# Optimization experiments

Measured on AMD Instinct MI355X. Metric: run time of the kernel, lower is better.

Reference implementation:

```python
import jax, jax.numpy as jnp
import numpy as np

# Fixed average-trace buffer from the module (length 120)
AVG = jnp.asarray([0.0256,0.0823,0.1157,0.1315,0.1366,0.1369,0.1347,0.1308,0.1259,0.1205,0.1146,0.1086,0.1028,0.097,0.0913,0.0858,0.0805,0.0756,0.0708,0.0664,0.0623,0.0584,0.0549,0.0515,0.0485,0.0456,0.0429,0.0404,0.0381,0.036,0.034,0.0321,0.0304,0.0287,0.0272,0.0258,0.0245,0.0233,0.0222,0.0211,0.0201,0.0191,0.0182,0.0173,0.0165,0.0158,0.015,0.0143,0.0137,0.013,0.0125,0.0119,0.0114,0.0108,0.0104,0.0099,0.0095,0.0091,0.0087,0.0083,0.008,0.0077,0.0074,0.0071,0.0068,0.0065,0.0062,0.006,0.0058,0.0055,0.0053,0.005,0.0049,0.0047,0.0045,0.0044,0.0042,0.004,0.0039,0.0038,0.0036,0.0034,0.0033,0.0032,0.0031,0.003,0.0029,0.0028,0.0027,0.0026,0.0025,0.0024,0.0023,0.0022,0.0021,0.0021,0.002,0.0019,0.0018,0.0018,0.0017,0.0017,0.0016,0.0016,0.0015,0.0015,0.0014,0.0014,0.0013,0.0013,0.0013,0.0012,0.0012,0.0011,0.0011,0.0011,0.001,0.001,0.001,0.0009], dtype=jnp.float32)


def _lstm(x, w_ih, w_hh, b):
    """PyTorch-semantics single-layer LSTM. x: [N,T,D], w_ih: [4H,D], w_hh: [4H,H], b: [4H] (= b_ih + b_hh). Gate order i,f,g,o."""
    xp = jnp.einsum('ntd,gd->ntg', x, w_ih) + b  # precompute input projections: [N,T,4H]
    N = x.shape[0]
    H = w_hh.shape[1]
    h0 = jnp.zeros((N, H), x.dtype)

    def step(carry, xt):
        h, c = carry
        g = xt + h @ w_hh.T  # [N,4H]
        i, f, gg, o = jnp.split(g, 4, axis=-1)
        c = jax.nn.sigmoid(f) * c + jax.nn.sigmoid(i) * jnp.tanh(gg)
        h = jax.nn.sigmoid(o) * jnp.tanh(c)
        return (h, c), h

    _, hs = jax.lax.scan(step, (h0, h0), jnp.swapaxes(xp, 0, 1))  # hs: [T,N,H]
    return jnp.swapaxes(hs, 0, 1)  # [N,T,H]


def setup_inputs() -> dict:
    key = jax.random.key(0)
    ks = jax.random.split(key, 7)
    N, F, H = 32768, 12, 30
    s1 = 1.0 / float(np.sqrt(H))  # torch LSTM init: U(-1/sqrt(H), 1/sqrt(H))
    s2 = 1.0                      # second LSTM hidden=1 -> scale 1
    return {
        'features': jax.random.normal(ks[0], (N, F), jnp.float32),
        'w_ih1': jax.random.uniform(ks[1], (4 * H, F + 1), jnp.float32, -s1, s1),
        'w_hh1': jax.random.uniform(ks[2], (4 * H, H), jnp.float32, -s1, s1),
        'b1': jax.random.uniform(ks[3], (4 * H,), jnp.float32, -s1, s1),
        'w_ih2': jax.random.uniform(ks[4], (4, H), jnp.float32, -s2, s2),
        'w_hh2': jax.random.uniform(ks[5], (4, 1), jnp.float32, -s2, s2),
        'b2': jax.random.uniform(ks[6], (4,), jnp.float32, -s2, s2),
    }


def reference(features, w_ih1, w_hh1, b1, w_ih2, w_hh2, b2):
    N, F = features.shape
    T = AVG.shape[0]  # 120
    x = jnp.broadcast_to(features[:, None, :], (N, T, F))          # repeat features over time
    trace = jnp.broadcast_to(AVG[None, :, None], (N, T, 1))        # average trace channel
    x = jnp.concatenate([x, trace], axis=2)                        # [N,120,13]
    h1 = _lstm(x, w_ih1, w_hh1, b1)                                # [N,120,30]
    return _lstm(h1, w_ih2, w_hh2, b2)                             # [N,120,1]
```

## Files before the change

kernel.cpp:

```cpp
#include <hip/hip_runtime.h>

typedef __attribute__((ext_vector_type(8))) short bf16x8;
typedef __attribute__((ext_vector_type(4))) float f32x4;

#define LOG2E 1.44269504088896340736f

__device__ __constant__ float AVG_D[120] = {
    0.0256f,0.0823f,0.1157f,0.1315f,0.1366f,0.1369f,0.1347f,0.1308f,0.1259f,0.1205f,
    0.1146f,0.1086f,0.1028f,0.0970f,0.0913f,0.0858f,0.0805f,0.0756f,0.0708f,0.0664f,
    0.0623f,0.0584f,0.0549f,0.0515f,0.0485f,0.0456f,0.0429f,0.0404f,0.0381f,0.0360f,
    0.0340f,0.0321f,0.0304f,0.0287f,0.0272f,0.0258f,0.0245f,0.0233f,0.0222f,0.0211f,
    0.0201f,0.0191f,0.0182f,0.0173f,0.0165f,0.0158f,0.0150f,0.0143f,0.0137f,0.0130f,
    0.0125f,0.0119f,0.0114f,0.0108f,0.0104f,0.0099f,0.0095f,0.0091f,0.0087f,0.0083f,
    0.0080f,0.0077f,0.0074f,0.0071f,0.0068f,0.0065f,0.0062f,0.0060f,0.0058f,0.0055f,
    0.0053f,0.0050f,0.0049f,0.0047f,0.0045f,0.0044f,0.0042f,0.0040f,0.0039f,0.0038f,
    0.0036f,0.0034f,0.0033f,0.0032f,0.0031f,0.0030f,0.0029f,0.0028f,0.0027f,0.0026f,
    0.0025f,0.0024f,0.0023f,0.0022f,0.0021f,0.0021f,0.0020f,0.0019f,0.0018f,0.0018f,
    0.0017f,0.0017f,0.0016f,0.0016f,0.0015f,0.0015f,0.0014f,0.0014f,0.0013f,0.0013f,
    0.0013f,0.0012f,0.0012f,0.0011f,0.0011f,0.0011f,0.0010f,0.0010f,0.0010f,0.0009f
};

__device__ __forceinline__ float sig2(float x) {
    return __builtin_amdgcn_rcpf(1.0f + __builtin_amdgcn_exp2f(x));
}
__device__ __forceinline__ float tanh2(float x) {
    return fmaf(2.0f, __builtin_amdgcn_rcpf(1.0f + __builtin_amdgcn_exp2f(x)), -1.0f);
}
__device__ __forceinline__ unsigned short tb(float x) {
    return (unsigned short)(__float_as_uint(x) >> 16);
}
__device__ __forceinline__ float fb(unsigned short h) {
    return __uint_as_float(((unsigned)h) << 16);
}

__device__ __forceinline__ void swap32(unsigned &a, unsigned &b) {
    auto r = __builtin_amdgcn_permlane32_swap(a, b, false, false);
    a = r[0]; b = r[1];
}
__device__ __forceinline__ void swap16(unsigned &a, unsigned &b) {
    auto r = __builtin_amdgcn_permlane16_swap(a, b, false, false);
    a = r[0]; b = r[1];
}

__global__ void pack_weights(const float* __restrict__ w_ih1,
                             const float* __restrict__ w_hh1,
                             const float* __restrict__ b1,
                             const float* __restrict__ w_ih2,
                             const float* __restrict__ b2,
                             float* __restrict__ ws) {
    unsigned short* whi = (unsigned short*)ws;
    unsigned short* wlo = (unsigned short*)(ws + 2048);
    float* bconst = ws + 4096;
    float* wih1f  = ws + 4224;
    unsigned* avgpk = (unsigned*)(ws + 5760);
    const int tid = threadIdx.x;
    for (int idx = tid; idx < 4096; idx += 256) {
        const int T = idx >> 9, lane = (idx >> 3) & 63, j = idx & 7;
        const int r = 16 * T + (lane & 15);
        const int k = ((lane >> 4) & 3) * 8 + j;
        const int u = r >> 2, q = r & 3;
        const float sc = (q == 2) ? (-2.0f * LOG2E) : (-LOG2E);
        float v = 0.0f;
        if (u < 30) {
            if (k < 30)       v = w_hh1[(q * 30 + u) * 30 + k];
            else if (k == 30) v = w_ih1[(q * 30 + u) * 13 + 12];
        } else if (u == 30 && k < 30) {
            v = w_ih2[q * 30 + k];
        }
        v *= sc;
        const unsigned short hi = tb(v);
        whi[idx] = hi;
        wlo[idx] = tb(v - fb(hi));
    }
    for (int r = tid; r < 128; r += 256) {
        const int u = r >> 2, q = r & 3;
        const float sc = (q == 2) ? (-2.0f * LOG2E) : (-LOG2E);
        bconst[r] = sc * ((u < 30) ? b1[q * 30 + u] : ((u == 30) ? b2[q] : 0.0f));
    }
    for (int idx = tid; idx < 1536; idx += 256) {
        const int r = idx / 12, d = idx % 12;
        const int u = r >> 2, q = r & 3;
        const float sc = (q == 2) ? (-2.0f * LOG2E) : (-LOG2E);
        wih1f[idx] = (u < 30) ? sc * w_ih1[(q * 30 + u) * 13 + d] : 0.0f;
    }
    for (int t = tid; t < 121; t += 256) {
        const float a = (t < 120) ? AVG_D[t] : 0.0f;
        const unsigned short hi = tb(a);
        const unsigned short lo = tb(a - fb(hi));
        avgpk[t] = (unsigned)hi | ((unsigned)lo << 16);
    }
}

__global__ __launch_bounds__(128, 2)
void lstm_mfma_kernel(const float* __restrict__ feat,
                      const float* __restrict__ w_hh2,
                      const float* __restrict__ ws,
                      float* __restrict__ out) {
    __shared__ __align__(16) float out_s[32 * 124];

    const int tid  = threadIdx.x;
    const int lane = tid & 63;
    const int wv   = __builtin_amdgcn_readfirstlane(tid >> 6);
    const int s    = lane & 15;
    const int quad = lane >> 4;
    const int seq  = blockIdx.x * 32 + wv * 16 + s;
    const unsigned* avgpk = (const unsigned*)(ws + 5760);

    bf16x8 Ahi[8], Alo[8];
    {
        const unsigned short* whi = (const unsigned short*)ws;
        const unsigned short* wlo = (const unsigned short*)(ws + 2048);
#pragma unroll
        for (int T = 0; T < 8; T++) {
            Ahi[T] = *(const bf16x8*)(whi + T * 512 + lane * 8);
            Alo[T] = *(const bf16x8*)(wlo + T * 512 + lane * 8);
        }
    }

    float f0[12];
    {
        const float4* fp = reinterpret_cast<const float4*>(feat + seq * 12);
        float4 A = fp[0], B = fp[1], C = fp[2];
        f0[0]=A.x; f0[1]=A.y; f0[2]=A.z; f0[3]=A.w;
        f0[4]=B.x; f0[5]=B.y; f0[6]=B.z; f0[7]=B.w;
        f0[8]=C.x; f0[9]=C.y; f0[10]=C.z; f0[11]=C.w;
    }
    f32x4 projb[8];
    {
        const float* bconst = ws + 4096;
        const float* wih1f  = ws + 4224;
#pragma unroll
        for (int T = 0; T < 8; T++) {
#pragma unroll
            for (int g = 0; g < 4; g++) {
                const int r = 16 * T + 4 * quad + g;
                float acc = bconst[r];
#pragma unroll
                for (int d = 0; d < 12; d++) acc = fmaf(f0[d], wih1f[r * 12 + d], acc);
                projb[T][g] = acc;
            }
        }
    }

    float c1[8];
#pragma unroll
    for (int T = 0; T < 8; T++) c1[T] = 0.0f;
    float h2 = 0.0f, c2 = 0.0f;
    const float whs0 = -LOG2E * w_hh2[0];
    const float whs1 = -LOG2E * w_hh2[1];
    const float whs2 = -2.0f * LOG2E * w_hh2[2];
    const float whs3 = -LOG2E * w_hh2[3];

    unsigned e0 = 0u, e1 = 0u, e2 = 0u, e3 = 0u;
    unsigned o0 = 0u, o1 = 0u, o2 = 0u, o3 = 0u;
    if (quad == 3) o2 = avgpk[0];
    union { int4 i; bf16x8 v; } ubh, ubl;
#define BUILD_B() do {                                                  \
        ubh.i.x = (int)__builtin_amdgcn_perm(e1, e0, 0x05040100u);      \
        ubh.i.y = (int)__builtin_amdgcn_perm(e3, e2, 0x05040100u);      \
        ubh.i.z = (int)__builtin_amdgcn_perm(o1, o0, 0x05040100u);      \
        ubh.i.w = (int)__builtin_amdgcn_perm(o3, o2, 0x05040100u);      \
        ubl.i.x = (int)__builtin_amdgcn_perm(e1, e0, 0x07060302u);      \
        ubl.i.y = (int)__builtin_amdgcn_perm(e3, e2, 0x07060302u);      \
        ubl.i.z = (int)__builtin_amdgcn_perm(o1, o0, 0x07060302u);      \
        ubl.i.w = (int)__builtin_amdgcn_perm(o3, o2, 0x07060302u);      \
    } while (0)
    BUILD_B();

    unsigned apk_cur = avgpk[1];

#pragma unroll 1
    for (int t = 0; t <= 120; t++) {
        const bf16x8 Bhi = ubh.v, Blo = ubl.v;

        const unsigned apk = apk_cur;
        apk_cur = avgpk[(t + 2 <= 120) ? (t + 2) : 120];

        f32x4 D[8];
#pragma unroll
        for (int T = 0; T < 8; T++)
            D[T] = __builtin_amdgcn_mfma_f32_16x16x32_bf16(Alo[T], Bhi, projb[T], 0, 0, 0);
#pragma unroll
        for (int T = 0; T < 8; T++)
            D[T] = __builtin_amdgcn_mfma_f32_16x16x32_bf16(Ahi[T], Blo, D[T], 0, 0, 0);
#pragma unroll
        for (int T = 0; T < 8; T++)
            D[T] = __builtin_amdgcn_mfma_f32_16x16x32_bf16(Ahi[T], Bhi, D[T], 0, 0, 0);

        if (t >= 1 && quad == 2) {
            const float g0 = fmaf(h2, whs0, D[7][0]);
            const float g1 = fmaf(h2, whs1, D[7][1]);
            const float g2 = fmaf(h2, whs2, D[7][2]);
            const float g3 = fmaf(h2, whs3, D[7][3]);
            c2 = sig2(g1) * c2 + sig2(g0) * tanh2(g2);
            h2 = sig2(g3) * tanh2(c2 * (-2.0f * LOG2E));
            out_s[(wv * 16 + s) * 124 + (t - 1)] = h2;
        }

        if (t < 120) {
            unsigned hpk[8];
#pragma unroll
            for (int T = 0; T < 8; T++) {
                const int u = 4 * T + quad;
                unsigned v = 0u;
                if (u < 30) {
                    const float ei = __builtin_amdgcn_exp2f(D[T][0]);
                    const float ef = __builtin_amdgcn_exp2f(D[T][1]);
                    const float eg = __builtin_amdgcn_exp2f(D[T][2]);
                    const float eo = __builtin_amdgcn_exp2f(D[T][3]);
                    const float pi_ = 1.0f + ei, pf = 1.0f + ef;
                    const float pg  = 1.0f + eg, po = 1.0f + eo;
                    const float pig = pi_ * pg;
                    const float num = fmaf(c1[T], pig, (1.0f - eg) * pf);
                    const float ck  = num * __builtin_amdgcn_rcpf(pf * pig);
                    c1[T] = ck;
                    float carg = -2.0f * LOG2E * ck;
                    carg = fminf(fmaxf(carg, -80.0f), 80.0f);
                    const float ec = __builtin_amdgcn_exp2f(carg);
                    const float hk = (1.0f - ec) *
                                     __builtin_amdgcn_rcpf(po * (1.0f + ec));
                    const unsigned hbits = __float_as_uint(hk);
                    const float rem = hk - __uint_as_float(hbits & 0xffff0000u);
                    v = __builtin_amdgcn_perm(__float_as_uint(rem), hbits, 0x07060302u);
                }
                hpk[T] = v;
            }

            e0 = hpk[0]; e1 = hpk[2]; e2 = hpk[4]; e3 = hpk[6];
            o0 = hpk[1]; o1 = hpk[3]; o2 = hpk[5]; o3 = hpk[7];
            swap32(e0, e2); swap32(e1, e3);
            swap16(e0, e1); swap16(e2, e3);
            swap32(o0, o2); swap32(o1, o3);
            swap16(o0, o1); swap16(o2, o3);
            if (quad == 3) { o2 = apk; o3 = 0u; }
            BUILD_B();
        }
    }

    __syncthreads();
    float* outb = out + (size_t)blockIdx.x * 32 * 120;
#pragma unroll
    for (int it = 0; it < 8; it++) {
        const int fi = it * 128 + tid;
        if (fi < 960) {
            const int sq = fi / 30, j = fi % 30;
            const float4 v = *reinterpret_cast<const float4*>(&out_s[sq * 124 + j * 4]);
            *reinterpret_cast<float4*>(&outb[sq * 120 + j * 4]) = v;
        }
    }
}

extern "C" void kernel_launch(void* const* d_in, const int* in_sizes, int n_in,
                              void* d_out, int out_size, void* d_ws, size_t ws_size,
                              hipStream_t stream) {
    (void)in_sizes; (void)n_in; (void)out_size; (void)ws_size;
    const float* feat  = (const float*)d_in[0];
    const float* w_ih1 = (const float*)d_in[1];
    const float* w_hh1 = (const float*)d_in[2];
    const float* b1    = (const float*)d_in[3];
    const float* w_ih2 = (const float*)d_in[4];
    const float* w_hh2 = (const float*)d_in[5];
    const float* b2    = (const float*)d_in[6];
    float* ws  = (float*)d_ws;
    float* out = (float*)d_out;

    hipLaunchKernelGGL(pack_weights, dim3(1), dim3(256), 0, stream,
                       w_ih1, w_hh1, b1, w_ih2, b2, ws);
    hipLaunchKernelGGL(lstm_mfma_kernel, dim3(1024), dim3(128), 0, stream,
                       feat, w_hh2, ws, out);
}
```

Before: 290.4 us.

## Split LSTM gate tiles across two waves with LDS hidden-state exchange

Each block now handles 16 sequences instead of 32, and its two waves each compute half of the 8 gate tiles. The hidden state is exchanged each timestep through a double-buffered LDS array guarded by __syncthreads, replacing the in-register permlane swaps. This halves per-wave MFMA and transcendental work per step and raises the occupancy hint, shortening the serial critical path. In exchange it adds an LDS round trip and a block barrier on every one of the 120 steps.

```diff
diff --git a/kernel.cpp b/kernel.cpp
--- a/kernel.cpp
+++ b/kernel.cpp
@@ -31,15 +31,6 @@
 }
 __device__ __forceinline__ float fb(unsigned short h) {
     return __uint_as_float(((unsigned)h) << 16);
-}
-
-__device__ __forceinline__ void swap32(unsigned &a, unsigned &b) {
-    auto r = __builtin_amdgcn_permlane32_swap(a, b, false, false);
-    a = r[0]; b = r[1];
-}
-__device__ __forceinline__ void swap16(unsigned &a, unsigned &b) {
-    auto r = __builtin_amdgcn_permlane16_swap(a, b, false, false);
-    a = r[0]; b = r[1];
 }
 
 __global__ void pack_weights(const float* __restrict__ w_ih1,
@@ -91,29 +82,35 @@
     }
 }
 
-__global__ __launch_bounds__(128, 2)
+__global__ __launch_bounds__(128, 4)
 void lstm_mfma_kernel(const float* __restrict__ feat,
                       const float* __restrict__ w_hh2,
                       const float* __restrict__ ws,
                       float* __restrict__ out) {
-    __shared__ __align__(16) float out_s[32 * 124];
+    __shared__ __align__(16) unsigned hx[2][16 * 36];
+    __shared__ __align__(16) float out_s[16 * 124];
 
     const int tid  = threadIdx.x;
     const int lane = tid & 63;
     const int wv   = __builtin_amdgcn_readfirstlane(tid >> 6);
     const int s    = lane & 15;
     const int quad = lane >> 4;
-    const int seq  = blockIdx.x * 32 + wv * 16 + s;
+    const int seq  = blockIdx.x * 16 + s;
     const unsigned* avgpk = (const unsigned*)(ws + 5760);
 
-    bf16x8 Ahi[8], Alo[8];
+    for (int i = tid; i < 2 * 16 * 36; i += 128) (&hx[0][0])[i] = 0u;
+    __syncthreads();
+    if (tid < 16) hx[0][tid * 36 + 30] = avgpk[0];
+
+    bf16x8 Ahi[4], Alo[4];
     {
         const unsigned short* whi = (const unsigned short*)ws;
         const unsigned short* wlo = (const unsigned short*)(ws + 2048);
 #pragma unroll
-        for (int T = 0; T < 8; T++) {
-            Ahi[T] = *(const bf16x8*)(whi + T * 512 + lane * 8);
-            Alo[T] = *(const bf16x8*)(wlo + T * 512 + lane * 8);
+        for (int T = 0; T < 4; T++) {
+            const int Tg = 4 * wv + T;
+            Ahi[T] = *(const bf16x8*)(whi + Tg * 512 + lane * 8);
+            Alo[T] = *(const bf16x8*)(wlo + Tg * 512 + lane * 8);
         }
     }
 
@@ -125,15 +122,15 @@
         f0[4]=B.x; f0[5]=B.y; f0[6]=B.z; f0[7]=B.w;
         f0[8]=C.x; f0[9]=C.y; f0[10]=C.z; f0[11]=C.w;
     }
-    f32x4 projb[8];
+    f32x4 projb[4];
     {
         const float* bconst = ws + 4096;
         const float* wih1f  = ws + 4224;
 #pragma unroll
-        for (int T = 0; T < 8; T++) {
+        for (int T = 0; T < 4; T++) {
 #pragma unroll
             for (int g = 0; g < 4; g++) {
-                const int r = 16 * T + 4 * quad + g;
+                const int r = 16 * (4 * wv + T) + 4 * quad + g;
                 float acc = bconst[r];
 #pragma unroll
                 for (int d = 0; d < 12; d++) acc = fmaf(f0[d], wih1f[r * 12 + d], acc);
@@ -142,66 +139,65 @@
         }
     }
 
-    float c1[8];
-#pragma unroll
-    for (int T = 0; T < 8; T++) c1[T] = 0.0f;
+    float c1[4];
+#pragma unroll
+    for (int T = 0; T < 4; T++) c1[T] = 0.0f;
     float h2 = 0.0f, c2 = 0.0f;
     const float whs0 = -LOG2E * w_hh2[0];
     const float whs1 = -LOG2E * w_hh2[1];
     const float whs2 = -2.0f * LOG2E * w_hh2[2];
     const float whs3 = -LOG2E * w_hh2[3];
 
-    unsigned e0 = 0u, e1 = 0u, e2 = 0u, e3 = 0u;
-    unsigned o0 = 0u, o1 = 0u, o2 = 0u, o3 = 0u;
-    if (quad == 3) o2 = avgpk[0];
-    union { int4 i; bf16x8 v; } ubh, ubl;
-#define BUILD_B() do {                                                  \
-        ubh.i.x = (int)__builtin_amdgcn_perm(e1, e0, 0x05040100u);      \
-        ubh.i.y = (int)__builtin_amdgcn_perm(e3, e2, 0x05040100u);      \
-        ubh.i.z = (int)__builtin_amdgcn_perm(o1, o0, 0x05040100u);      \
-        ubh.i.w = (int)__builtin_amdgcn_perm(o3, o2, 0x05040100u);      \
-        ubl.i.x = (int)__builtin_amdgcn_perm(e1, e0, 0x07060302u);      \
-        ubl.i.y = (int)__builtin_amdgcn_perm(e3, e2, 0x07060302u);      \
-        ubl.i.z = (int)__builtin_amdgcn_perm(o1, o0, 0x07060302u);      \
-        ubl.i.w = (int)__builtin_amdgcn_perm(o3, o2, 0x07060302u);      \
-    } while (0)
-    BUILD_B();
+    __syncthreads();
 
     unsigned apk_cur = avgpk[1];
 
 #pragma unroll 1
     for (int t = 0; t <= 120; t++) {
-        const bf16x8 Bhi = ubh.v, Blo = ubl.v;
+        const unsigned* hb = hx[t & 1];
+        unsigned*       hn = hx[(t & 1) ^ 1];
 
         const unsigned apk = apk_cur;
         apk_cur = avgpk[(t + 2 <= 120) ? (t + 2) : 120];
 
-        f32x4 D[8];
-#pragma unroll
-        for (int T = 0; T < 8; T++)
+        const uint4 Ra = *reinterpret_cast<const uint4*>(hb + s * 36 + 8 * quad);
+        const uint4 Rb = *reinterpret_cast<const uint4*>(hb + s * 36 + 8 * quad + 4);
+        union { int4 i; bf16x8 v; } ubh, ubl;
+        ubh.i.x = (int)__builtin_amdgcn_perm(Ra.y, Ra.x, 0x05040100u);
+        ubh.i.y = (int)__builtin_amdgcn_perm(Ra.w, Ra.z, 0x05040100u);
+        ubh.i.z = (int)__builtin_amdgcn_perm(Rb.y, Rb.x, 0x05040100u);
+        ubh.i.w = (int)__builtin_amdgcn_perm(Rb.w, Rb.z, 0x05040100u);
+        ubl.i.x = (int)__builtin_amdgcn_perm(Ra.y, Ra.x, 0x07060302u);
+        ubl.i.y = (int)__builtin_amdgcn_perm(Ra.w, Ra.z, 0x07060302u);
+        ubl.i.z = (int)__builtin_amdgcn_perm(Rb.y, Rb.x, 0x07060302u);
+        ubl.i.w = (int)__builtin_amdgcn_perm(Rb.w, Rb.z, 0x07060302u);
+        const bf16x8 Bhi = ubh.v, Blo = ubl.v;
+
+        f32x4 D[4];
+#pragma unroll
+        for (int T = 0; T < 4; T++)
             D[T] = __builtin_amdgcn_mfma_f32_16x16x32_bf16(Alo[T], Bhi, projb[T], 0, 0, 0);
 #pragma unroll
-        for (int T = 0; T < 8; T++)
+        for (int T = 0; T < 4; T++)
             D[T] = __builtin_amdgcn_mfma_f32_16x16x32_bf16(Ahi[T], Blo, D[T], 0, 0, 0);
 #pragma unroll
-        for (int T = 0; T < 8; T++)
+        for (int T = 0; T < 4; T++)
             D[T] = __builtin_amdgcn_mfma_f32_16x16x32_bf16(Ahi[T], Bhi, D[T], 0, 0, 0);
 
-        if (t >= 1 && quad == 2) {
-            const float g0 = fmaf(h2, whs0, D[7][0]);
-            const float g1 = fmaf(h2, whs1, D[7][1]);
-            const float g2 = fmaf(h2, whs2, D[7][2]);
-            const float g3 = fmaf(h2, whs3, D[7][3]);
+        if (wv == 1 && t >= 1 && quad == 2) {
+            const float g0 = fmaf(h2, whs0, D[3][0]);
+            const float g1 = fmaf(h2, whs1, D[3][1]);
+            const float g2 = fmaf(h2, whs2, D[3][2]);
+            const float g3 = fmaf(h2, whs3, D[3][3]);
             c2 = sig2(g1) * c2 + sig2(g0) * tanh2(g2);
             h2 = sig2(g3) * tanh2(c2 * (-2.0f * LOG2E));
-            out_s[(wv * 16 + s) * 124 + (t - 1)] = h2;
+            out_s[s * 124 + (t - 1)] = h2;
         }
 
         if (t < 120) {
-            unsigned hpk[8];
-#pragma unroll
-            for (int T = 0; T < 8; T++) {
-                const int u = 4 * T + quad;
+#pragma unroll
+            for (int T = 0; T < 4; T++) {
+                const int u = 16 * wv + 4 * T + quad;
                 unsigned v = 0u;
                 if (u < 30) {
                     const float ei = __builtin_amdgcn_exp2f(D[T][0]);
@@ -222,27 +218,21 @@
                     const unsigned hbits = __float_as_uint(hk);
                     const float rem = hk - __uint_as_float(hbits & 0xffff0000u);
                     v = __builtin_amdgcn_perm(__float_as_uint(rem), hbits, 0x07060302u);
+                } else if (u == 30) {
+                    v = apk;
                 }
-                hpk[T] = v;
+                hn[s * 36 + u] = v;
             }
-
-            e0 = hpk[0]; e1 = hpk[2]; e2 = hpk[4]; e3 = hpk[6];
-            o0 = hpk[1]; o1 = hpk[3]; o2 = hpk[5]; o3 = hpk[7];
-            swap32(e0, e2); swap32(e1, e3);
-            swap16(e0, e1); swap16(e2, e3);
-            swap32(o0, o2); swap32(o1, o3);
-            swap16(o0, o1); swap16(o2, o3);
-            if (quad == 3) { o2 = apk; o3 = 0u; }
-            BUILD_B();
+            __syncthreads();
         }
     }
 
     __syncthreads();
-    float* outb = out + (size_t)blockIdx.x * 32 * 120;
-#pragma unroll
-    for (int it = 0; it < 8; it++) {
+    float* outb = out + (size_t)blockIdx.x * 16 * 120;
+#pragma unroll
+    for (int it = 0; it < 4; it++) {
         const int fi = it * 128 + tid;
-        if (fi < 960) {
+        if (fi < 480) {
             const int sq = fi / 30, j = fi % 30;
             const float4 v = *reinterpret_cast<const float4*>(&out_s[sq * 124 + j * 4]);
             *reinterpret_cast<float4*>(&outb[sq * 120 + j * 4]) = v;
@@ -266,6 +256,6 @@
 
     hipLaunchKernelGGL(pack_weights, dim3(1), dim3(256), 0, stream,
                        w_ih1, w_hh1, b1, w_ih2, b2, ws);
-    hipLaunchKernelGGL(lstm_mfma_kernel, dim3(1024), dim3(128), 0, stream,
+    hipLaunchKernelGGL(lstm_mfma_kernel, dim3(2048), dim3(128), 0, stream,
                        feat, w_hh2, ws, out);
 }
```

After: 257.3 us. 1.13x faster.
